# Kernel tuning notes

Measured on AMD Instinct MI355X. Metric: run time of the kernel, lower is better.

Reference implementation:

```python
import jax, jax.numpy as jnp
import numpy as np

B, S, D, H = 1, 4096, 1024, 16
HD = D // H  # head_dim = 64


def setup_inputs() -> dict:
    key = jax.random.key(0)
    ks = jax.random.split(key, 5)
    scale = 1.0 / np.sqrt(D)
    return {
        "x_self": jax.random.normal(ks[0], (B, S, D), dtype=jnp.float32),
        "W_q": jax.random.normal(ks[1], (D, D), dtype=jnp.float32) * scale,
        "W_k": jax.random.normal(ks[2], (D, D), dtype=jnp.float32) * scale,
        "W_v": jax.random.normal(ks[3], (D, D), dtype=jnp.float32) * scale,
        "W_o": jax.random.normal(ks[4], (D, D), dtype=jnp.float32) * scale,
    }


def reference(x_self, W_q, W_k, W_v, W_o):
    b, s, d = x_self.shape
    # nn.Linear(bias=False): y = x @ W.T
    q = x_self @ W_q.T
    k = x_self @ W_k.T
    v = x_self @ W_v.T
    # [b, h, s, hd]
    q = q.reshape(b, s, H, HD).transpose(0, 2, 1, 3)
    k = k.reshape(b, s, H, HD).transpose(0, 2, 1, 3)
    v = v.reshape(b, s, H, HD).transpose(0, 2, 1, 3)
    scores = jnp.einsum("bhqd,bhkd->bhqk", q, k) / jnp.sqrt(jnp.float32(HD))
    # causal mask: -inf strictly above diagonal
    causal = jnp.triu(jnp.full((s, s), -jnp.inf, dtype=scores.dtype), k=1)
    scores = scores + causal[None, None, :, :]
    attn = jax.nn.softmax(scores.astype(jnp.float32), axis=-1).astype(q.dtype)
    ctx = jnp.einsum("bhqk,bhkd->bhqd", attn, v)  # [b, h, s, hd]
    out = ctx.transpose(0, 2, 1, 3).reshape(b, s, d)
    return out @ W_o.T
```

## Files before the change

kernel.cpp:

```cpp
#include <hip/hip_runtime.h>

typedef unsigned short u16;
typedef unsigned int u32;
typedef __attribute__((ext_vector_type(8))) short s16x8;
typedef __attribute__((ext_vector_type(4))) short s16x4;
typedef __attribute__((ext_vector_type(4))) float f32x4;

#define S_LEN 4096
#define D_DIM 1024
#define NH    16
#define HDIM  64
#define KVB   128
#define QB    128

#define AS1 __attribute__((address_space(1)))
#define AS3 __attribute__((address_space(3)))

__device__ __forceinline__ u16 f2bf(float f) {
  unsigned u = __float_as_uint(f);
  u += 0x7FFF + ((u >> 16) & 1);
  return (u16)(u >> 16);
}

__device__ __forceinline__ u32 cvtpk2(float a, float b) {
  float r;
  asm("v_cvt_pk_bf16_f32 %0, %1, %2" : "=v"(r) : "v"(a), "v"(b));
  return __float_as_uint(r);
}

__device__ __forceinline__ u16 f2bf_pk(float f) {
  return (u16)(cvtpk2(f, f) & 0xffffu);
}

__device__ __forceinline__ float exp2fast(float x) {
  float r;
  asm("v_exp_f32 %0, %1" : "=v"(r) : "v"(x));
  return r;
}

__device__ __forceinline__ void load_lds16(const void* g, void* l) {
  __builtin_amdgcn_global_load_lds((AS1 void*)g, (AS3 void*)l, 16, 0, 0);
}

__device__ __forceinline__ unsigned lds_addr32(const void* p) {
  return (unsigned)(unsigned long long)(AS3 const char*)p;
}

__device__ __forceinline__ s16x4 ds_read_tr16(unsigned addr) {
  s16x4 r;
  asm volatile("ds_read_b64_tr_b16 %0, %1" : "=v"(r) : "v"(addr));
  return r;
}

__global__ __launch_bounds__(256) void cvt_all(const float* __restrict__ x,
                                               const float* __restrict__ w0,
                                               const float* __restrict__ w1,
                                               const float* __restrict__ w2,
                                               const float* __restrict__ w3,
                                               u16* xb, u16* o0, u16* o1,
                                               u16* o2, u16* o3) {
  const float* in; u16* out;
  const int slab = blockIdx.y;
  switch (slab) {
    case 0: case 1: case 2: case 3:
      in = x + (size_t)slab * D_DIM * 1024; out = xb + (size_t)slab * D_DIM * 1024; break;
    case 4: in = w0; out = o0; break;
    case 5: in = w1; out = o1; break;
    case 6: in = w2; out = o2; break;
    default: in = w3; out = o3; break;
  }
  int i = (blockIdx.x * 256 + threadIdx.x) * 4;
  float4 v = *(const float4*)(in + i);
  ushort4 o;
  o.x = f2bf(v.x); o.y = f2bf(v.y); o.z = f2bf(v.z); o.w = f2bf(v.w);
  *(ushort4*)(out + i) = o;
}

struct GemmSmem { u16 As[2][128 * 32]; u16 Bs[2][128 * 32]; };

template <bool BF16_OUT>
__device__ __forceinline__ void gemm_tile(GemmSmem& sm, const u16* __restrict__ A,
                                          const u16* __restrict__ B,
                                          void* __restrict__ C, int m0, int n0,
                                          int N, int K, float cscale) {
  const int t = threadIdx.x;
  const int l = t & 63, g = l >> 4, r = l & 15;
  const int w = t >> 6, wr = w >> 1, wc = w & 1;
  f32x4 acc[4][4] = {};
  const int swz = (g ^ ((r >> 1) & 3)) << 3;

  auto stage = [&](int buf, int k0) {
#pragma unroll
    for (int i = 0; i < 2; ++i) {
      const int gi = i * 256 + t;
      const int row = gi >> 2, cg = gi & 3;
      const int sc = cg ^ ((row >> 1) & 3);
      load_lds16(A + (size_t)(m0 + row) * K + k0 + sc * 8,
                 (char*)sm.As[buf] + (i * 256 + (t & 192)) * 16);
      load_lds16(B + (size_t)(n0 + row) * K + k0 + sc * 8,
                 (char*)sm.Bs[buf] + (i * 256 + (t & 192)) * 16);
    }
  };

  stage(0, 0);
  __syncthreads();
  int cur = 0;
  for (int k0 = 0; k0 < K; k0 += 32) {
    if (k0 + 32 < K) stage(cur ^ 1, k0 + 32);
    s16x8 a[4], b[4];
#pragma unroll
    for (int m = 0; m < 4; ++m)
      a[m] = *(const s16x8*)&sm.As[cur][(wr * 64 + m * 16 + r) * 32 + swz];
#pragma unroll
    for (int n = 0; n < 4; ++n)
      b[n] = *(const s16x8*)&sm.Bs[cur][(wc * 64 + n * 16 + r) * 32 + swz];
#pragma unroll
    for (int m = 0; m < 4; ++m)
#pragma unroll
      for (int n = 0; n < 4; ++n)
        acc[m][n] = __builtin_amdgcn_mfma_f32_16x16x32_bf16(a[m], b[n], acc[m][n], 0, 0, 0);
    __syncthreads();
    cur ^= 1;
  }
#pragma unroll
  for (int m = 0; m < 4; ++m)
#pragma unroll
    for (int n = 0; n < 4; ++n)
#pragma unroll
      for (int v = 0; v < 4; ++v) {
        int row = m0 + wr * 64 + m * 16 + g * 4 + v;
        int col = n0 + wc * 64 + n * 16 + r;
        float val = acc[m][n][v] * cscale;
        if (BF16_OUT)
          ((u16*)C)[(size_t)row * N + col] = f2bf_pk(val);
        else
          ((float*)C)[(size_t)row * N + col] = val;
      }
}

#define QSCALE 0.1803368801111204f

__global__ __launch_bounds__(256) void gemm_qkv(const u16* __restrict__ A,
                                                const u16* __restrict__ Bq,
                                                const u16* __restrict__ Bk,
                                                const u16* __restrict__ Bv,
                                                u16* Cq, u16* Ck, u16* Cv_) {
  __shared__ GemmSmem sm;
  const int f = blockIdx.y * 24 + blockIdx.x;
  const int tid = (f & 7) * 96 + (f >> 3);
  const int nby = tid / 24, nbx = tid % 24;
  const int which = nbx >> 3;
  const u16* B = which == 0 ? Bq : (which == 1 ? Bk : Bv);
  u16* C = which == 0 ? Cq : (which == 1 ? Ck : Cv_);
  const float cs = which == 0 ? QSCALE : 1.0f;
  gemm_tile<true>(sm, A, B, C, nby * 128, (nbx & 7) * 128, D_DIM, D_DIM, cs);
}

__global__ __launch_bounds__(256) void gemm_out(const u16* __restrict__ A,
                                                const u16* __restrict__ B,
                                                float* __restrict__ C) {
  __shared__ GemmSmem sm;
  const int f = blockIdx.y * 8 + blockIdx.x;
  const int tid = (f & 7) * 32 + (f >> 3);
  gemm_tile<false>(sm, A, B, C, (tid >> 3) * 128, (tid & 7) * 128, D_DIM, D_DIM, 1.0f);
}

__global__ __launch_bounds__(512) void flash_attn(const u16* __restrict__ Q,
                                                  const u16* __restrict__ Kg,
                                                  const u16* __restrict__ V,
                                                  u16* __restrict__ CTX) {
  const int h = blockIdx.y;
  const int hoff = h * HDIM;
  const int t = threadIdx.x, w = t >> 6, l = t & 63, g = l >> 4, r = l & 15;

  __shared__ u16 Kt[2][KVB * 64];
  __shared__ u16 Vt[2][32 * 256];

  auto stage = [&](int buf, int kv0) {
#pragma unroll
    for (int i = 0; i < 2; ++i) {
      const int gi = i * 512 + t;
      const int krow = gi >> 3, c0 = gi & 7;
      load_lds16(Kg + (size_t)(kv0 + krow) * D_DIM + hoff + ((c0 ^ (krow & 7)) << 3),
                 (char*)Kt[buf] + (i * 512 + (t & 448)) * 16);
      const int sv = gi >> 5, vo = gi & 31;
      load_lds16(V + (size_t)(kv0 + (sv >> 2) * 16 + (vo >> 1)) * D_DIM + hoff +
                     (sv & 3) * 16 + (vo & 1) * 8,
                 (char*)Vt[buf] + (i * 512 + (t & 448)) * 16);
    }
  };

#pragma unroll 1
  for (int run = 0; run < 2; ++run) {
    const int qt = run == 0 ? (31 - (int)blockIdx.x) : (int)blockIdx.x;
    const int q0 = qt * QB + w * 16;

    const u16* qrow = Q + (size_t)(q0 + r) * D_DIM + hoff;
    const s16x8 aq0 = *(const s16x8*)(qrow + g * 8);
    const s16x8 aq1 = *(const s16x8*)(qrow + 32 + g * 8);

    f32x4 o[4] = {};
    float mrun = -1e30f, lsum = 0.f;

    const int ntiles = qt + 1;
    stage(0, 0);
    __syncthreads();
    int cur = 0;

    for (int tile = 0; tile < ntiles; ++tile) {
      if (tile + 1 < ntiles) stage(cur ^ 1, (tile + 1) * KVB);
      const u16* Kb = Kt[cur];
      const bool lastT = (tile == ntiles - 1);

      f32x4 s[8];
      __builtin_amdgcn_s_setprio(1);
#pragma unroll
      for (int nb = 0; nb < 8; ++nb) {
        const int kr = nb * 16 + r;
        const int sw = kr & 7;
        s16x8 bk0 = *(const s16x8*)&Kb[kr * 64 + ((g ^ sw) << 3)];
        s16x8 bk1 = *(const s16x8*)&Kb[kr * 64 + (((4 + g) ^ sw) << 3)];
        f32x4 z = {0.f, 0.f, 0.f, 0.f};
        z = __builtin_amdgcn_mfma_f32_16x16x32_bf16(bk0, aq0, z, 0, 0, 0);
        z = __builtin_amdgcn_mfma_f32_16x16x32_bf16(bk1, aq1, z, 0, 0, 0);
        s[nb] = z;
      }
      __builtin_amdgcn_s_setprio(0);

      if (lastT) {
        const int qrel = q0 + r - tile * KVB;
#pragma unroll
        for (int nb = 0; nb < 8; ++nb)
#pragma unroll
          for (int j = 0; j < 4; ++j)
            if (16 * nb + 4 * g + j > qrel) s[nb][j] = -1e30f;
      }

      float tm = -1e30f;
#pragma unroll
      for (int nb = 0; nb < 8; ++nb) {
        float a0 = fmaxf(s[nb][0], s[nb][1]), a1 = fmaxf(s[nb][2], s[nb][3]);
        tm = fmaxf(tm, fmaxf(a0, a1));
      }
      tm = fmaxf(tm, __shfl_xor(tm, 16, 64));
      tm = fmaxf(tm, __shfl_xor(tm, 32, 64));
      const float mnew = fmaxf(mrun, tm);
      const float fs = exp2fast(mrun - mnew);
      mrun = mnew;
      float ps = 0.f;
#pragma unroll
      for (int nb = 0; nb < 8; ++nb)
#pragma unroll
        for (int j = 0; j < 4; ++j) {
          const float pv = exp2fast(s[nb][j] - mnew);
          s[nb][j] = pv;
          ps += pv;
        }
      ps += __shfl_xor(ps, 16, 64);
      ps += __shfl_xor(ps, 32, 64);
      lsum = lsum * fs + ps;
#pragma unroll
      for (int hb = 0; hb < 4; ++hb) {
        o[hb][0] *= fs; o[hb][1] *= fs; o[hb][2] *= fs; o[hb][3] *= fs;
      }

      s16x8 pa[4];
#pragma unroll
      for (int ks = 0; ks < 4; ++ks) {
        union { u32 u[4]; s16x8 v; } pk_;
        pk_.u[0] = cvtpk2(s[2 * ks][0],     s[2 * ks][1]);
        pk_.u[1] = cvtpk2(s[2 * ks][2],     s[2 * ks][3]);
        pk_.u[2] = cvtpk2(s[2 * ks + 1][0], s[2 * ks + 1][1]);
        pk_.u[3] = cvtpk2(s[2 * ks + 1][2], s[2 * ks + 1][3]);
        pa[ks] = pk_.v;
      }

      const unsigned vbase = lds_addr32(Vt[cur]) + (unsigned)(l * 8);
      s16x4 tv[4][4][2];
      auto issue_grp = [&](int ks) {
#pragma unroll
        for (int hb = 0; hb < 4; ++hb) {
          tv[ks][hb][0] = ds_read_tr16(vbase + (unsigned)(((2 * ks) * 4 + hb) * 512));
          tv[ks][hb][1] = ds_read_tr16(vbase + (unsigned)(((2 * ks + 1) * 4 + hb) * 512));
        }
      };
      issue_grp(0);
      issue_grp(1);
#pragma unroll
      for (int ks = 0; ks < 4; ++ks) {
        if (ks < 3) asm volatile("s_waitcnt lgkmcnt(8)" ::: "memory");
        else        asm volatile("s_waitcnt lgkmcnt(0)" ::: "memory");
        __builtin_amdgcn_sched_barrier(0);
        __builtin_amdgcn_s_setprio(1);
#pragma unroll
        for (int hb = 0; hb < 4; ++hb) {
          s16x8 vf = {tv[ks][hb][0][0], tv[ks][hb][0][1], tv[ks][hb][0][2], tv[ks][hb][0][3],
                      tv[ks][hb][1][0], tv[ks][hb][1][1], tv[ks][hb][1][2], tv[ks][hb][1][3]};
          o[hb] = __builtin_amdgcn_mfma_f32_16x16x32_bf16(vf, pa[ks], o[hb], 0, 0, 0);
        }
        __builtin_amdgcn_s_setprio(0);
        if (ks < 2) issue_grp(ks + 2);
      }
      __syncthreads();
      cur ^= 1;
    }

    const float inv = 1.0f / lsum;
    u16* crow = CTX + (size_t)(q0 + r) * D_DIM + hoff + 4 * g;
#pragma unroll
    for (int hb = 0; hb < 4; ++hb) {
      uint2 pk_;
      pk_.x = cvtpk2(o[hb][0] * inv, o[hb][1] * inv);
      pk_.y = cvtpk2(o[hb][2] * inv, o[hb][3] * inv);
      *(uint2*)(crow + hb * 16) = pk_;
    }
  }
}

extern "C" void kernel_launch(void* const* d_in, const int* in_sizes, int n_in,
                              void* d_out, int out_size, void* d_ws, size_t ws_size,
                              hipStream_t stream) {
  const float* x  = (const float*)d_in[0];
  const float* Wq = (const float*)d_in[1];
  const float* Wk = (const float*)d_in[2];
  const float* Wv = (const float*)d_in[3];
  const float* Wo = (const float*)d_in[4];

  u16* xb  = (u16*)d_ws;
  u16* Wqb = xb + (size_t)S_LEN * D_DIM;
  u16* Wkb = Wqb + (size_t)D_DIM * D_DIM;
  u16* Wvb = Wkb + (size_t)D_DIM * D_DIM;
  u16* Wob = Wvb + (size_t)D_DIM * D_DIM;
  u16* Qb  = Wob + (size_t)D_DIM * D_DIM;
  u16* Kb  = Qb + (size_t)S_LEN * D_DIM;
  u16* Vb  = Kb + (size_t)S_LEN * D_DIM;
  u16* Cb  = Vb + (size_t)S_LEN * D_DIM;

  cvt_all<<<dim3(1024, 8), 256, 0, stream>>>(x, Wq, Wk, Wv, Wo,
                                             xb, Wqb, Wkb, Wvb, Wob);
  gemm_qkv<<<dim3(24, 32), 256, 0, stream>>>(xb, Wqb, Wkb, Wvb, Qb, Kb, Vb);
  flash_attn<<<dim3(S_LEN / QB / 2, NH), 512, 0, stream>>>(Qb, Kb, Vb, Cb);
  gemm_out<<<dim3(8, 32), 256, 0, stream>>>(Cb, Wob, (float*)d_out);
}
```

Measured before the change: 203.3 us.

## Triple-buffer K/V tiles and compute next tile's QK^T before current softmax

Expands the K/V shared-memory ring from two to three buffers and prefetches two tiles ahead. Each iteration now issues the QK^T MFMAs for the next tile before the softmax and PV of the current one, ping-ponging two score register sets. This lets matrix-core work overlap the exp/max VALU work and hides more global load latency. In exchange it uses 50% more LDS and extra score registers, which may lower occupancy or cause spills.

```diff
diff --git a/kernel.cpp b/kernel.cpp
--- a/kernel.cpp
+++ b/kernel.cpp
@@ -173,8 +173,8 @@
   const int hoff = h * HDIM;
   const int t = threadIdx.x, w = t >> 6, l = t & 63, g = l >> 4, r = l & 15;
 
-  __shared__ u16 Kt[2][KVB * 64];
-  __shared__ u16 Vt[2][32 * 256];
+  __shared__ u16 Kt[3][KVB * 64];
+  __shared__ u16 Vt[3][32 * 256];
 
   auto stage = [&](int buf, int kv0) {
 #pragma unroll
@@ -194,6 +194,7 @@
   for (int run = 0; run < 2; ++run) {
     const int qt = run == 0 ? (31 - (int)blockIdx.x) : (int)blockIdx.x;
     const int q0 = qt * QB + w * 16;
+    const int nt = qt + 1;
 
     const u16* qrow = Q + (size_t)(q0 + r) * D_DIM + hoff;
     const s16x8 aq0 = *(const s16x8*)(qrow + g * 8);
@@ -201,19 +202,9 @@
 
     f32x4 o[4] = {};
     float mrun = -1e30f, lsum = 0.f;
-
-    const int ntiles = qt + 1;
-    stage(0, 0);
-    __syncthreads();
-    int cur = 0;
-
-    for (int tile = 0; tile < ntiles; ++tile) {
-      if (tile + 1 < ntiles) stage(cur ^ 1, (tile + 1) * KVB);
-      const u16* Kb = Kt[cur];
-      const bool lastT = (tile == ntiles - 1);
-
-      f32x4 s[8];
-      __builtin_amdgcn_s_setprio(1);
+    int b0 = 0, b1 = 1, b2 = 2;
+
+    auto qk = [&](const u16* Kb, f32x4 (&sd)[8]) {
 #pragma unroll
       for (int nb = 0; nb < 8; ++nb) {
         const int kr = nb * 16 + r;
@@ -223,23 +214,27 @@
         f32x4 z = {0.f, 0.f, 0.f, 0.f};
         z = __builtin_amdgcn_mfma_f32_16x16x32_bf16(bk0, aq0, z, 0, 0, 0);
         z = __builtin_amdgcn_mfma_f32_16x16x32_bf16(bk1, aq1, z, 0, 0, 0);
-        s[nb] = z;
-      }
-      __builtin_amdgcn_s_setprio(0);
-
-      if (lastT) {
-        const int qrel = q0 + r - tile * KVB;
+        sd[nb] = z;
+      }
+    };
+
+    auto step = [&](int tt, f32x4 (&sC)[8], f32x4 (&sN)[8]) {
+      if (tt + 2 < nt) stage(b2, (tt + 2) * KVB);
+      if (tt + 1 < nt) qk(Kt[b1], sN);
+
+      if (tt == nt - 1) {
+        const int qrel = q0 + r - tt * KVB;
 #pragma unroll
         for (int nb = 0; nb < 8; ++nb)
 #pragma unroll
           for (int j = 0; j < 4; ++j)
-            if (16 * nb + 4 * g + j > qrel) s[nb][j] = -1e30f;
+            if (16 * nb + 4 * g + j > qrel) sC[nb][j] = -1e30f;
       }
 
       float tm = -1e30f;
 #pragma unroll
       for (int nb = 0; nb < 8; ++nb) {
-        float a0 = fmaxf(s[nb][0], s[nb][1]), a1 = fmaxf(s[nb][2], s[nb][3]);
+        float a0 = fmaxf(sC[nb][0], sC[nb][1]), a1 = fmaxf(sC[nb][2], sC[nb][3]);
         tm = fmaxf(tm, fmaxf(a0, a1));
       }
       tm = fmaxf(tm, __shfl_xor(tm, 16, 64));
@@ -252,8 +247,8 @@
       for (int nb = 0; nb < 8; ++nb)
 #pragma unroll
         for (int j = 0; j < 4; ++j) {
-          const float pv = exp2fast(s[nb][j] - mnew);
-          s[nb][j] = pv;
+          const float pv = exp2fast(sC[nb][j] - mnew);
+          sC[nb][j] = pv;
           ps += pv;
         }
       ps += __shfl_xor(ps, 16, 64);
@@ -268,14 +263,14 @@
 #pragma unroll
       for (int ks = 0; ks < 4; ++ks) {
         union { u32 u[4]; s16x8 v; } pk_;
-        pk_.u[0] = cvtpk2(s[2 * ks][0],     s[2 * ks][1]);
-        pk_.u[1] = cvtpk2(s[2 * ks][2],     s[2 * ks][3]);
-        pk_.u[2] = cvtpk2(s[2 * ks + 1][0], s[2 * ks + 1][1]);
-        pk_.u[3] = cvtpk2(s[2 * ks + 1][2], s[2 * ks + 1][3]);
+        pk_.u[0] = cvtpk2(sC[2 * ks][0],     sC[2 * ks][1]);
+        pk_.u[1] = cvtpk2(sC[2 * ks][2],     sC[2 * ks][3]);
+        pk_.u[2] = cvtpk2(sC[2 * ks + 1][0], sC[2 * ks + 1][1]);
+        pk_.u[3] = cvtpk2(sC[2 * ks + 1][2], sC[2 * ks + 1][3]);
         pa[ks] = pk_.v;
       }
 
-      const unsigned vbase = lds_addr32(Vt[cur]) + (unsigned)(l * 8);
+      const unsigned vbase = lds_addr32(Vt[b0]) + (unsigned)(l * 8);
       s16x4 tv[4][4][2];
       auto issue_grp = [&](int ks) {
 #pragma unroll
@@ -302,7 +297,19 @@
         if (ks < 2) issue_grp(ks + 2);
       }
       __syncthreads();
-      cur ^= 1;
+      const int tmp = b0; b0 = b1; b1 = b2; b2 = tmp;
+    };
+
+    stage(b0, 0);
+    if (nt > 1) stage(b1, KVB);
+    __syncthreads();
+    f32x4 sA[8], sB[8];
+    qk(Kt[b0], sA);
+
+    for (int tt = 0; tt < nt; ) {
+      step(tt, sA, sB); ++tt;
+      if (tt >= nt) break;
+      step(tt, sB, sA); ++tt;
     }
 
     const float inv = 1.0f / lsum;
```

Measured after the change: 210.7 us. 1.04x slower.

## Give each attention wave two 16-row query strips and launch one block per q-tile

Applied to the files above, without the earlier changes.

The flash-attention kernel moves from 8 waves of 16 query rows that each process two q-tiles in sequence to 4 waves of 32 query rows (two interleaved 16-row strips), with one block per q-tile and a grid of 32x16. Each K and V fragment read from LDS now feeds two MFMAs, halving LDS read traffic per unit of work and giving more independent MFMA chains for latency hiding. The grid doubles to 512 blocks, ordered longest tile first. The costs are higher register pressure from doubled accumulators and score tiles, fewer waves per block to share each staged K/V tile, and no pairing of short and long tiles within a block, so per-block work is less balanced.

```diff
diff --git a/kernel.cpp b/kernel.cpp
--- a/kernel.cpp
+++ b/kernel.cpp
@@ -165,7 +165,7 @@
   gemm_tile<false>(sm, A, B, C, (tid >> 3) * 128, (tid & 7) * 128, D_DIM, D_DIM, 1.0f);
 }
 
-__global__ __launch_bounds__(512) void flash_attn(const u16* __restrict__ Q,
+__global__ __launch_bounds__(256) void flash_attn(const u16* __restrict__ Q,
                                                   const u16* __restrict__ Kg,
                                                   const u16* __restrict__ V,
                                                   u16* __restrict__ CTX) {
@@ -178,142 +178,166 @@
 
   auto stage = [&](int buf, int kv0) {
 #pragma unroll
-    for (int i = 0; i < 2; ++i) {
-      const int gi = i * 512 + t;
+    for (int i = 0; i < 4; ++i) {
+      const int gi = i * 256 + t;
       const int krow = gi >> 3, c0 = gi & 7;
       load_lds16(Kg + (size_t)(kv0 + krow) * D_DIM + hoff + ((c0 ^ (krow & 7)) << 3),
-                 (char*)Kt[buf] + (i * 512 + (t & 448)) * 16);
+                 (char*)Kt[buf] + (i * 256 + (t & 192)) * 16);
       const int sv = gi >> 5, vo = gi & 31;
       load_lds16(V + (size_t)(kv0 + (sv >> 2) * 16 + (vo >> 1)) * D_DIM + hoff +
                      (sv & 3) * 16 + (vo & 1) * 8,
-                 (char*)Vt[buf] + (i * 512 + (t & 448)) * 16);
+                 (char*)Vt[buf] + (i * 256 + (t & 192)) * 16);
     }
   };
 
-#pragma unroll 1
-  for (int run = 0; run < 2; ++run) {
-    const int qt = run == 0 ? (31 - (int)blockIdx.x) : (int)blockIdx.x;
-    const int q0 = qt * QB + w * 16;
-
-    const u16* qrow = Q + (size_t)(q0 + r) * D_DIM + hoff;
-    const s16x8 aq0 = *(const s16x8*)(qrow + g * 8);
-    const s16x8 aq1 = *(const s16x8*)(qrow + 32 + g * 8);
-
-    f32x4 o[4] = {};
-    float mrun = -1e30f, lsum = 0.f;
-
-    const int ntiles = qt + 1;
-    stage(0, 0);
-    __syncthreads();
-    int cur = 0;
-
-    for (int tile = 0; tile < ntiles; ++tile) {
-      if (tile + 1 < ntiles) stage(cur ^ 1, (tile + 1) * KVB);
-      const u16* Kb = Kt[cur];
-      const bool lastT = (tile == ntiles - 1);
-
-      f32x4 s[8];
+  const int bx = (int)blockIdx.x;
+  const int qtile = bx < 16 ? 31 - bx : bx - 16;
+  const int q0 = qtile * QB + w * 32;
+  const int nt = qtile + 1;
+
+  const u16* qrowA = Q + (size_t)(q0 + r) * D_DIM + hoff;
+  const u16* qrowB = qrowA + 16 * D_DIM;
+  const s16x8 aqA0 = *(const s16x8*)(qrowA + g * 8);
+  const s16x8 aqA1 = *(const s16x8*)(qrowA + 32 + g * 8);
+  const s16x8 aqB0 = *(const s16x8*)(qrowB + g * 8);
+  const s16x8 aqB1 = *(const s16x8*)(qrowB + 32 + g * 8);
+
+  f32x4 oA[4] = {}, oB[4] = {};
+  float mA = -1e30f, lsA = 0.f, mB = -1e30f, lsB = 0.f;
+
+  stage(0, 0);
+  __syncthreads();
+  int cur = 0;
+
+  for (int tile = 0; tile < nt; ++tile) {
+    if (tile + 1 < nt) stage(cur ^ 1, (tile + 1) * KVB);
+    const u16* Kb = Kt[cur];
+    const bool lastT = (tile == nt - 1);
+
+    f32x4 sA[8], sB[8];
+    __builtin_amdgcn_s_setprio(1);
+#pragma unroll
+    for (int nb = 0; nb < 8; ++nb) {
+      const int kr = nb * 16 + r;
+      const int sw = kr & 7;
+      s16x8 bk0 = *(const s16x8*)&Kb[kr * 64 + ((g ^ sw) << 3)];
+      s16x8 bk1 = *(const s16x8*)&Kb[kr * 64 + (((4 + g) ^ sw) << 3)];
+      f32x4 zA = {0.f, 0.f, 0.f, 0.f}, zB = {0.f, 0.f, 0.f, 0.f};
+      zA = __builtin_amdgcn_mfma_f32_16x16x32_bf16(bk0, aqA0, zA, 0, 0, 0);
+      zB = __builtin_amdgcn_mfma_f32_16x16x32_bf16(bk0, aqB0, zB, 0, 0, 0);
+      zA = __builtin_amdgcn_mfma_f32_16x16x32_bf16(bk1, aqA1, zA, 0, 0, 0);
+      zB = __builtin_amdgcn_mfma_f32_16x16x32_bf16(bk1, aqB1, zB, 0, 0, 0);
+      sA[nb] = zA; sB[nb] = zB;
+    }
+    __builtin_amdgcn_s_setprio(0);
+
+    if (lastT) {
+      const int qrelA = w * 32 + r;
+      const int qrelB = qrelA + 16;
+#pragma unroll
+      for (int nb = 0; nb < 8; ++nb)
+#pragma unroll
+        for (int j = 0; j < 4; ++j) {
+          const int kvl = 16 * nb + 4 * g + j;
+          if (kvl > qrelA) sA[nb][j] = -1e30f;
+          if (kvl > qrelB) sB[nb][j] = -1e30f;
+        }
+    }
+
+    float tmA = -1e30f, tmB = -1e30f;
+#pragma unroll
+    for (int nb = 0; nb < 8; ++nb) {
+      tmA = fmaxf(tmA, fmaxf(fmaxf(sA[nb][0], sA[nb][1]), fmaxf(sA[nb][2], sA[nb][3])));
+      tmB = fmaxf(tmB, fmaxf(fmaxf(sB[nb][0], sB[nb][1]), fmaxf(sB[nb][2], sB[nb][3])));
+    }
+    tmA = fmaxf(tmA, __shfl_xor(tmA, 16, 64));
+    tmA = fmaxf(tmA, __shfl_xor(tmA, 32, 64));
+    tmB = fmaxf(tmB, __shfl_xor(tmB, 16, 64));
+    tmB = fmaxf(tmB, __shfl_xor(tmB, 32, 64));
+    const float mnA = fmaxf(mA, tmA), mnB = fmaxf(mB, tmB);
+    const float fsA = exp2fast(mA - mnA), fsB = exp2fast(mB - mnB);
+    mA = mnA; mB = mnB;
+    float psA = 0.f, psB = 0.f;
+#pragma unroll
+    for (int nb = 0; nb < 8; ++nb)
+#pragma unroll
+      for (int j = 0; j < 4; ++j) {
+        const float pA = exp2fast(sA[nb][j] - mnA);
+        const float pB = exp2fast(sB[nb][j] - mnB);
+        sA[nb][j] = pA; sB[nb][j] = pB;
+        psA += pA; psB += pB;
+      }
+    psA += __shfl_xor(psA, 16, 64);
+    psA += __shfl_xor(psA, 32, 64);
+    psB += __shfl_xor(psB, 16, 64);
+    psB += __shfl_xor(psB, 32, 64);
+    lsA = lsA * fsA + psA;
+    lsB = lsB * fsB + psB;
+#pragma unroll
+    for (int hb = 0; hb < 4; ++hb) {
+      oA[hb][0] *= fsA; oA[hb][1] *= fsA; oA[hb][2] *= fsA; oA[hb][3] *= fsA;
+      oB[hb][0] *= fsB; oB[hb][1] *= fsB; oB[hb][2] *= fsB; oB[hb][3] *= fsB;
+    }
+
+    s16x8 paA[4], paB[4];
+#pragma unroll
+    for (int ks = 0; ks < 4; ++ks) {
+      union { u32 u[4]; s16x8 v; } pk_;
+      pk_.u[0] = cvtpk2(sA[2 * ks][0],     sA[2 * ks][1]);
+      pk_.u[1] = cvtpk2(sA[2 * ks][2],     sA[2 * ks][3]);
+      pk_.u[2] = cvtpk2(sA[2 * ks + 1][0], sA[2 * ks + 1][1]);
+      pk_.u[3] = cvtpk2(sA[2 * ks + 1][2], sA[2 * ks + 1][3]);
+      paA[ks] = pk_.v;
+      pk_.u[0] = cvtpk2(sB[2 * ks][0],     sB[2 * ks][1]);
+      pk_.u[1] = cvtpk2(sB[2 * ks][2],     sB[2 * ks][3]);
+      pk_.u[2] = cvtpk2(sB[2 * ks + 1][0], sB[2 * ks + 1][1]);
+      pk_.u[3] = cvtpk2(sB[2 * ks + 1][2], sB[2 * ks + 1][3]);
+      paB[ks] = pk_.v;
+    }
+
+    const unsigned vbase = lds_addr32(Vt[cur]) + (unsigned)(l * 8);
+    s16x4 tv[4][4][2];
+    auto issue_grp = [&](int ks) {
+#pragma unroll
+      for (int hb = 0; hb < 4; ++hb) {
+        tv[ks][hb][0] = ds_read_tr16(vbase + (unsigned)(((2 * ks) * 4 + hb) * 512));
+        tv[ks][hb][1] = ds_read_tr16(vbase + (unsigned)(((2 * ks + 1) * 4 + hb) * 512));
+      }
+    };
+    issue_grp(0);
+    issue_grp(1);
+#pragma unroll
+    for (int ks = 0; ks < 4; ++ks) {
+      if (ks < 3) asm volatile("s_waitcnt lgkmcnt(8)" ::: "memory");
+      else        asm volatile("s_waitcnt lgkmcnt(0)" ::: "memory");
+      __builtin_amdgcn_sched_barrier(0);
       __builtin_amdgcn_s_setprio(1);
 #pragma unroll
-      for (int nb = 0; nb < 8; ++nb) {
-        const int kr = nb * 16 + r;
-        const int sw = kr & 7;
-        s16x8 bk0 = *(const s16x8*)&Kb[kr * 64 + ((g ^ sw) << 3)];
-        s16x8 bk1 = *(const s16x8*)&Kb[kr * 64 + (((4 + g) ^ sw) << 3)];
-        f32x4 z = {0.f, 0.f, 0.f, 0.f};
-        z = __builtin_amdgcn_mfma_f32_16x16x32_bf16(bk0, aq0, z, 0, 0, 0);
-        z = __builtin_amdgcn_mfma_f32_16x16x32_bf16(bk1, aq1, z, 0, 0, 0);
-        s[nb] = z;
+      for (int hb = 0; hb < 4; ++hb) {
+        s16x8 vf = {tv[ks][hb][0][0], tv[ks][hb][0][1], tv[ks][hb][0][2], tv[ks][hb][0][3],
+                    tv[ks][hb][1][0], tv[ks][hb][1][1], tv[ks][hb][1][2], tv[ks][hb][1][3]};
+        oA[hb] = __builtin_amdgcn_mfma_f32_16x16x32_bf16(vf, paA[ks], oA[hb], 0, 0, 0);
+        oB[hb] = __builtin_amdgcn_mfma_f32_16x16x32_bf16(vf, paB[ks], oB[hb], 0, 0, 0);
       }
       __builtin_amdgcn_s_setprio(0);
-
-      if (lastT) {
-        const int qrel = q0 + r - tile * KVB;
-#pragma unroll
-        for (int nb = 0; nb < 8; ++nb)
-#pragma unroll
-          for (int j = 0; j < 4; ++j)
-            if (16 * nb + 4 * g + j > qrel) s[nb][j] = -1e30f;
-      }
-
-      float tm = -1e30f;
-#pragma unroll
-      for (int nb = 0; nb < 8; ++nb) {
-        float a0 = fmaxf(s[nb][0], s[nb][1]), a1 = fmaxf(s[nb][2], s[nb][3]);
-        tm = fmaxf(tm, fmaxf(a0, a1));
-      }
-      tm = fmaxf(tm, __shfl_xor(tm, 16, 64));
-      tm = fmaxf(tm, __shfl_xor(tm, 32, 64));
-      const float mnew = fmaxf(mrun, tm);
-      const float fs = exp2fast(mrun - mnew);
-      mrun = mnew;
-      float ps = 0.f;
-#pragma unroll
-      for (int nb = 0; nb < 8; ++nb)
-#pragma unroll
-        for (int j = 0; j < 4; ++j) {
-          const float pv = exp2fast(s[nb][j] - mnew);
-          s[nb][j] = pv;
-          ps += pv;
-        }
-      ps += __shfl_xor(ps, 16, 64);
-      ps += __shfl_xor(ps, 32, 64);
-      lsum = lsum * fs + ps;
-#pragma unroll
-      for (int hb = 0; hb < 4; ++hb) {
-        o[hb][0] *= fs; o[hb][1] *= fs; o[hb][2] *= fs; o[hb][3] *= fs;
-      }
-
-      s16x8 pa[4];
-#pragma unroll
-      for (int ks = 0; ks < 4; ++ks) {
-        union { u32 u[4]; s16x8 v; } pk_;
-        pk_.u[0] = cvtpk2(s[2 * ks][0],     s[2 * ks][1]);
-        pk_.u[1] = cvtpk2(s[2 * ks][2],     s[2 * ks][3]);
-        pk_.u[2] = cvtpk2(s[2 * ks + 1][0], s[2 * ks + 1][1]);
-        pk_.u[3] = cvtpk2(s[2 * ks + 1][2], s[2 * ks + 1][3]);
-        pa[ks] = pk_.v;
-      }
-
-      const unsigned vbase = lds_addr32(Vt[cur]) + (unsigned)(l * 8);
-      s16x4 tv[4][4][2];
-      auto issue_grp = [&](int ks) {
-#pragma unroll
-        for (int hb = 0; hb < 4; ++hb) {
-          tv[ks][hb][0] = ds_read_tr16(vbase + (unsigned)(((2 * ks) * 4 + hb) * 512));
-          tv[ks][hb][1] = ds_read_tr16(vbase + (unsigned)(((2 * ks + 1) * 4 + hb) * 512));
-        }
-      };
-      issue_grp(0);
-      issue_grp(1);
-#pragma unroll
-      for (int ks = 0; ks < 4; ++ks) {
-        if (ks < 3) asm volatile("s_waitcnt lgkmcnt(8)" ::: "memory");
-        else        asm volatile("s_waitcnt lgkmcnt(0)" ::: "memory");
-        __builtin_amdgcn_sched_barrier(0);
-        __builtin_amdgcn_s_setprio(1);
-#pragma unroll
-        for (int hb = 0; hb < 4; ++hb) {
-          s16x8 vf = {tv[ks][hb][0][0], tv[ks][hb][0][1], tv[ks][hb][0][2], tv[ks][hb][0][3],
-                      tv[ks][hb][1][0], tv[ks][hb][1][1], tv[ks][hb][1][2], tv[ks][hb][1][3]};
-          o[hb] = __builtin_amdgcn_mfma_f32_16x16x32_bf16(vf, pa[ks], o[hb], 0, 0, 0);
-        }
-        __builtin_amdgcn_s_setprio(0);
-        if (ks < 2) issue_grp(ks + 2);
-      }
-      __syncthreads();
-      cur ^= 1;
-    }
-
-    const float inv = 1.0f / lsum;
-    u16* crow = CTX + (size_t)(q0 + r) * D_DIM + hoff + 4 * g;
-#pragma unroll
-    for (int hb = 0; hb < 4; ++hb) {
-      uint2 pk_;
-      pk_.x = cvtpk2(o[hb][0] * inv, o[hb][1] * inv);
-      pk_.y = cvtpk2(o[hb][2] * inv, o[hb][3] * inv);
-      *(uint2*)(crow + hb * 16) = pk_;
-    }
+      if (ks < 2) issue_grp(ks + 2);
+    }
+    __syncthreads();
+    cur ^= 1;
+  }
+
+  const float invA = 1.0f / lsA, invB = 1.0f / lsB;
+  u16* crowA = CTX + (size_t)(q0 + r) * D_DIM + hoff + 4 * g;
+  u16* crowB = crowA + 16 * D_DIM;
+#pragma unroll
+  for (int hb = 0; hb < 4; ++hb) {
+    uint2 pkA, pkB;
+    pkA.x = cvtpk2(oA[hb][0] * invA, oA[hb][1] * invA);
+    pkA.y = cvtpk2(oA[hb][2] * invA, oA[hb][3] * invA);
+    pkB.x = cvtpk2(oB[hb][0] * invB, oB[hb][1] * invB);
+    pkB.y = cvtpk2(oB[hb][2] * invB, oB[hb][3] * invB);
+    *(uint2*)(crowA + hb * 16) = pkA;
+    *(uint2*)(crowB + hb * 16) = pkB;
   }
 }
 
@@ -339,6 +363,6 @@
   cvt_all<<<dim3(1024, 8), 256, 0, stream>>>(x, Wq, Wk, Wv, Wo,
                                              xb, Wqb, Wkb, Wvb, Wob);
   gemm_qkv<<<dim3(24, 32), 256, 0, stream>>>(xb, Wqb, Wkb, Wvb, Qb, Kb, Vb);
-  flash_attn<<<dim3(S_LEN / QB / 2, NH), 512, 0, stream>>>(Qb, Kb, Vb, Cb);
+  flash_attn<<<dim3(32, NH), 256, 0, stream>>>(Qb, Kb, Vb, Cb);
   gemm_out<<<dim3(8, 32), 256, 0, stream>>>(Cb, Wob, (float*)d_out);
 }
```

New measurement: 243.4 us. 19.7% more time.
